# Kernel tuning notes

Hardware: AMD Instinct MI355X
Metric: run time of the kernel (lower is better)

The kernel has to match this reference:

```python
import math
import jax, jax.numpy as jnp
import numpy as np

B, N, D, NH, DFF, DRAW, TMAX = 4, 1024, 512, 8, 2048, 32, 2
DK = D // NH
LN_EPS = 1e-5


def bayes_linear(x, w_mu, w_rho, b_mu, b_rho):
    # closed-form mean/variance of a variational linear layer
    w_sig = jax.nn.softplus(w_rho)
    b_sig = jax.nn.softplus(b_rho)
    mean = x @ w_mu.T + b_mu
    var = (x * x) @ (w_sig * w_sig).T + b_sig * b_sig
    return mean, var


def layer_norm(x, g, b):
    mu = jnp.mean(x, axis=-1, keepdims=True)
    v = jnp.var(x, axis=-1, keepdims=True)
    return (x - mu) / jnp.sqrt(v + LN_EPS) * g + b


def gelu_deriv(x):
    phi = 0.5 * (1.0 + jax.lax.erf(x / math.sqrt(2.0)))
    pdf = jnp.exp(-0.5 * x * x) / math.sqrt(2.0 * math.pi)
    return phi + x * pdf


def attention(x, x_raw, w_mu, w_rho, b_mu, b_rho, log_sigma_f, log_length):
    Bb, Nn, Dd = x.shape
    qm, _ = bayes_linear(x, w_mu[0], w_rho[0], b_mu[0], b_rho[0])
    km, _ = bayes_linear(x, w_mu[1], w_rho[1], b_mu[1], b_rho[1])
    vm, vv = bayes_linear(x, w_mu[2], w_rho[2], b_mu[2], b_rho[2])

    def heads(t):
        return t.reshape(Bb, Nn, NH, DK).transpose(0, 2, 1, 3)  # [B,H,N,dk]

    Q, K, V, Vv = heads(qm), heads(km), heads(vm), heads(vv)
    scores = jnp.einsum('bhnd,bhmd->bhnm', Q, K) / math.sqrt(DK)
    # RBF kernel on raw inputs, per head; dist2 via |x|^2+|x'|^2-2xx' (no [B,N,N,d] diff tensor)
    sq = jnp.sum(x_raw * x_raw, axis=-1)
    dist2 = jnp.maximum(sq[:, :, None] + sq[:, None, :] - 2.0 * jnp.einsum('bnd,bmd->bnm', x_raw, x_raw), 0.0)
    sigma_f2 = jnp.exp(2.0 * log_sigma_f)
    length2 = jnp.exp(2.0 * log_length)
    rbf = sigma_f2[None, :, None, None] * jnp.exp(-dist2[:, None, :, :] / (2.0 * length2[None, :, None, None]))
    attn = jax.nn.softmax(scores + rbf, axis=-1)
    ctx = jnp.einsum('bhnm,bhmd->bhnd', attn, V).transpose(0, 2, 1, 3).reshape(Bb, Nn, Dd)
    vta = jnp.einsum('bhnm,bhmd->bhnd', attn * attn, Vv).transpose(0, 2, 1, 3).reshape(Bb, Nn, Dd)
    om, ovp = bayes_linear(ctx, w_mu[3], w_rho[3], b_mu[3], b_rho[3])
    return om, ovp + vta


def ffn(x, w1_mu, w1_rho, b1_mu, b1_rho, w2_mu, w2_rho, b2_mu, b2_rho):
    hm, hv = bayes_linear(x, w1_mu, w1_rho, b1_mu, b1_rho)
    am = jax.nn.gelu(hm, approximate=False)
    av = gelu_deriv(hm) ** 2 * hv
    om, ovd = bayes_linear(am, w2_mu, w2_rho, b2_mu, b2_rho)
    w2_sig = jax.nn.softplus(w2_rho)
    vc = av @ (w2_mu * w2_mu + w2_sig * w2_sig).T
    return om, ovd + vc


def cascade(H, H_var, tau_k, x_raw, attn_w_mu, attn_w_rho, attn_b_mu, attn_b_rho,
            w1_mu, w1_rho, b1_mu, b1_rho, w2_mu, w2_rho, b2_mu, b2_rho,
            ln1_g, ln1_b, ln2_g, ln2_b, log_sigma_f, log_length, log_gammas):
    g = jax.nn.softplus(log_gammas)
    g1, g2, g3, g4 = g[0], g[1], g[2], g[3]
    alpha = g1 / (g1 + g2)  # E[alpha] (inference path)
    beta = g3 / (g3 + g4)
    Va = g1 * g2 / ((g1 + g2) ** 2 * (g1 + g2 + 1.0))
    Vb = g3 * g4 / ((g3 + g4) ** 2 * (g3 + g4 + 1.0))
    done = jnp.asarray(False)
    for _ in range(TMAX):
        n1 = layer_norm(H, ln1_g, ln1_b)
        am, avar = attention(n1, x_raw, attn_w_mu, attn_w_rho, attn_b_mu, attn_b_rho, log_sigma_f, log_length)
        Hb = H + am
        n2 = layer_norm(Hb, ln2_g, ln2_b)
        fm, fvar = ffn(n2, w1_mu, w1_rho, b1_mu, b1_rho, w2_mu, w2_rho, b2_mu, b2_rho)
        F_out = Hb + fm
        F_var = avar + fvar
        Hn = alpha * H + beta * F_out
        Hvn = (alpha ** 2) * H_var + (beta ** 2) * F_var + Va * H * H + Vb * F_out * F_out + Va * H_var + Vb * F_var
        H = jnp.where(done, H, Hn)
        H_var = jnp.where(done, H_var, Hvn)
        done = done | (jnp.mean(H_var) <= tau_k)  # early-exit freeze
    return H, H_var


def setup_inputs() -> dict:
    key = jax.random.key(0)
    ks = jax.random.split(key, 8)
    inp = {
        'H': jax.random.normal(ks[0], (B, N, D), jnp.float32),
        'H_var': jax.random.uniform(ks[1], (B, N, D), jnp.float32) * 0.1,
        'x_raw': jax.random.normal(ks[2], (B, N, DRAW), jnp.float32) * 0.15,
        'tau_k': jnp.zeros((), jnp.float32),
        'attn_w_mu': jax.random.normal(ks[3], (4, D, D), jnp.float32) / math.sqrt(D),
        'attn_w_rho': jnp.full((4, D, D), -3.0, jnp.float32),
        'attn_b_mu': jnp.zeros((4, D), jnp.float32),
        'attn_b_rho': jnp.full((4, D), -3.0, jnp.float32),
        'w1_mu': jax.random.normal(ks[4], (DFF, D), jnp.float32) / math.sqrt(D),
        'w1_rho': jnp.full((DFF, D), -3.0, jnp.float32),
        'b1_mu': jnp.zeros((DFF,), jnp.float32),
        'b1_rho': jnp.full((DFF,), -3.0, jnp.float32),
        'w2_mu': jax.random.normal(ks[5], (D, DFF), jnp.float32) / math.sqrt(DFF),
        'w2_rho': jnp.full((D, DFF), -3.0, jnp.float32),
        'b2_mu': jnp.zeros((D,), jnp.float32),
        'b2_rho': jnp.full((D,), -3.0, jnp.float32),
        'ln1_g': jnp.ones((D,), jnp.float32),
        'ln1_b': jnp.zeros((D,), jnp.float32),
        'ln2_g': jnp.ones((D,), jnp.float32),
        'ln2_b': jnp.zeros((D,), jnp.float32),
        'log_sigma_f': jnp.zeros((NH,), jnp.float32),
        'log_length': jnp.zeros((NH,), jnp.float32),
        'log_gammas': jnp.ones((4,), jnp.float32),
    }
    return inp


def reference(H, H_var, x_raw, tau_k, attn_w_mu, attn_w_rho, attn_b_mu, attn_b_rho,
              w1_mu, w1_rho, b1_mu, b1_rho, w2_mu, w2_rho, b2_mu, b2_rho,
              ln1_g, ln1_b, ln2_g, ln2_b, log_sigma_f, log_length, log_gammas):
    return cascade(H, H_var, tau_k, x_raw, attn_w_mu, attn_w_rho, attn_b_mu, attn_b_rho,
                   w1_mu, w1_rho, b1_mu, b1_rho, w2_mu, w2_rho, b2_mu, b2_rho,
                   ln1_g, ln1_b, ln2_g, ln2_b, log_sigma_f, log_length, log_gammas)
```

## Files before the change

### kernel.cpp

```cpp
#include <hip/hip_runtime.h>
#include <math.h>


#define Bx   4
#define Nx   1024
#define Dx   512
#define NHx  8
#define DFFx 2048

static constexpr size_t BN  = (size_t)Bx * Nx;
static constexpr size_t BND = BN * Dx;
static constexpr size_t BNF = BN * DFFx;
static constexpr int    DD  = Dx * Dx;
static constexpr int    DF  = DFFx * Dx;

typedef __attribute__((ext_vector_type(8))) short bf16x8;
typedef __attribute__((ext_vector_type(4))) float f32x4;

__device__ __forceinline__ float sp_(float x) {
  return x > 20.f ? x : log1pf(expf(x));
}
__device__ __forceinline__ unsigned short f2b(float f) {
  unsigned u = __float_as_uint(f);
  unsigned r = (u + 0x7fffu + ((u >> 16) & 1u)) >> 16;
  return (unsigned short)r;
}
__device__ __forceinline__ float b2f(unsigned short v) {
  return __uint_as_float((unsigned)v << 16);
}
__device__ __forceinline__ void gld16(const void* g, void* l) {
  __builtin_amdgcn_global_load_lds(
      (const __attribute__((address_space(1))) unsigned int*)g,
      (__attribute__((address_space(3))) unsigned int*)l, 16, 0, 0);
}

__global__ __launch_bounds__(256) void cvt_weights(
    const float* __restrict__ aw_mu, const float* __restrict__ aw_rho,
    const float* __restrict__ w1_mu, const float* __restrict__ w1_rho,
    const float* __restrict__ w2_mu, const float* __restrict__ w2_rho,
    unsigned short* __restrict__ aw_bf,
    unsigned short* __restrict__ wvvar_bf,
    unsigned short* __restrict__ wovar_bf,
    unsigned short* __restrict__ w1_bf, unsigned short* __restrict__ w1var_bf,
    unsigned short* __restrict__ w2_bf, unsigned short* __restrict__ w2var_bf,
    unsigned short* __restrict__ w2comb_bf)
{
  int i = blockIdx.x * 256 + threadIdx.x;
  if (i < 4 * DD) {
    aw_bf[i] = f2b(aw_mu[i]);
  } else if (i < 6 * DD) {
    int j = i - 4 * DD;
    if (j < DD) { float s = sp_(aw_rho[2 * DD + j]); wvvar_bf[j] = f2b(s * s); }
    else { int k = j - DD; float s = sp_(aw_rho[3 * DD + k]); wovar_bf[k] = f2b(s * s); }
  } else if (i < 6 * DD + DF) {
    int j = i - 6 * DD;
    w1_bf[j] = f2b(w1_mu[j]);
  } else if (i < 6 * DD + 2 * DF) {
    int j = i - 6 * DD - DF;
    float s = sp_(w1_rho[j]); w1var_bf[j] = f2b(s * s);
  } else if (i < 6 * DD + 3 * DF) {
    int j = i - 6 * DD - 2 * DF;
    float m = w2_mu[j];
    float s = sp_(w2_rho[j]); float v = s * s;
    w2_bf[j] = f2b(m);
    w2var_bf[j] = f2b(v);
    w2comb_bf[j] = f2b(m * m + v);
  }
}

__global__ __launch_bounds__(256) void prep_small(
    const float* __restrict__ attn_b_rho, const float* __restrict__ b1_rho,
    const float* __restrict__ b2_rho, const float* __restrict__ xraw,
    float* __restrict__ bv2, float* __restrict__ bo2,
    float* __restrict__ b1v, float* __restrict__ b2v,
    float* __restrict__ sqb)
{
  int i = blockIdx.x * 256 + threadIdx.x;
  if (i < 512) {
    float s = sp_(attn_b_rho[1024 + i]); bv2[i] = s * s;
  } else if (i < 1024) {
    int k = i - 512;
    float s = sp_(attn_b_rho[1536 + k]); bo2[k] = s * s;
  } else if (i < 3072) {
    int k = i - 1024;
    float s = sp_(b1_rho[k]); b1v[k] = s * s;
  } else if (i < 3584) {
    int k = i - 3072;
    float s = sp_(b2_rho[k]); b2v[k] = s * s;
  } else if (i < 3584 + (int)BN) {
    int row = i - 3584;
    const float* x = xraw + (size_t)row * 32;
    float acc = 0.f;
    #pragma unroll
    for (int t = 0; t < 32; t++) acc += x[t] * x[t];
    sqb[row] = acc;
  }
}

__global__ __launch_bounds__(256) void gram_rbf(
    const float* __restrict__ xraw, const float* __restrict__ sqb,
    const float* __restrict__ lsf, const float* __restrict__ lll,
    unsigned short* __restrict__ rbf)
{
  const int nt = blockIdx.x, mt = blockIdx.y, b = blockIdx.z;
  __shared__ float xn[64][36];
  __shared__ float xm[64][36];
  __shared__ float sn[64], sm[64];
  const int tid = threadIdx.x;
  for (int q = tid; q < 512; q += 256) {
    int rr = q >> 3, cc = (q & 7) << 2;
    *(float4*)&xn[rr][cc] =
        *(const float4*)(xraw + ((size_t)b * Nx + nt * 64 + rr) * 32 + cc);
    *(float4*)&xm[rr][cc] =
        *(const float4*)(xraw + ((size_t)b * Nx + mt * 64 + rr) * 32 + cc);
  }
  if (tid < 64) {
    sn[tid] = sqb[(size_t)b * Nx + nt * 64 + tid];
    sm[tid] = sqb[(size_t)b * Nx + mt * 64 + tid];
  }
  __syncthreads();
  const int r = tid >> 2, j = tid & 3;
  float dd[16];
  #pragma unroll
  for (int i = 0; i < 16; i++) {
    int mm = j * 16 + i;
    float g = 0.f;
    #pragma unroll
    for (int t = 0; t < 32; t++) g += xn[r][t] * xm[mm][t];
    dd[i] = fmaxf(sn[r] + sm[mm] - 2.f * g, 0.f);
  }
  const int n = nt * 64 + r;
  #pragma unroll
  for (int h = 0; h < NHx; h++) {
    float sf2 = expf(2.f * lsf[h]);
    float i2l = 0.5f * expf(-2.f * lll[h]);
    unsigned short tmp[16];
    #pragma unroll
    for (int i = 0; i < 16; i++) tmp[i] = f2b(sf2 * expf(-dd[i] * i2l));
    unsigned short* dst =
        rbf + ((size_t)(h * Bx + b) * Nx + n) * Nx + mt * 64 + j * 16;
    *(uint4*)dst = *(const uint4*)&tmp[0];
    *(uint4*)(dst + 8) = *(const uint4*)&tmp[8];
  }
}

__global__ __launch_bounds__(256) void layernorm_bf(
    const float* __restrict__ X, const float* __restrict__ g,
    const float* __restrict__ bta,
    unsigned short* __restrict__ Y, unsigned short* __restrict__ Ysq)
{
  const int row = blockIdx.x;
  const float* x = X + (size_t)row * Dx;
  const int tid = threadIdx.x;
  float v0 = x[tid], v1 = x[tid + 256];
  float s = v0 + v1;
  float ss = v0 * v0 + v1 * v1;
  #pragma unroll
  for (int o = 32; o > 0; o >>= 1) {
    s += __shfl_down(s, o);
    ss += __shfl_down(ss, o);
  }
  __shared__ float ps[4], pss[4];
  const int w = tid >> 6;
  if ((tid & 63) == 0) { ps[w] = s; pss[w] = ss; }
  __syncthreads();
  float S = ps[0] + ps[1] + ps[2] + ps[3];
  float SS = pss[0] + pss[1] + pss[2] + pss[3];
  float mean = S * (1.f / 512.f);
  float var = fmaxf(SS * (1.f / 512.f) - mean * mean, 0.f);
  float inv = rsqrtf(var + 1e-5f);
  float y0 = (v0 - mean) * inv * g[tid] + bta[tid];
  float y1 = (v1 - mean) * inv * g[tid + 256] + bta[tid + 256];
  Y[(size_t)row * Dx + tid] = f2b(y0);
  Y[(size_t)row * Dx + tid + 256] = f2b(y1);
  Ysq[(size_t)row * Dx + tid] = f2b(y0 * y0);
  Ysq[(size_t)row * Dx + tid + 256] = f2b(y1 * y1);
}

struct GD {
  const unsigned short* A;
  const unsigned short* W;
  const float* bias;
  const float* add_in;
  void* C;
  int N;
  int trans;
};

template <bool HALFM, bool OUTBF>
__global__ __launch_bounds__(256) void gemm_mf(
    GD d0, GD d1, GD d2, int M, int K, int ldc)
{
  const GD d = (blockIdx.z == 0) ? d0 : ((blockIdx.z == 1) ? d1 : d2);
  const int n0 = blockIdx.x * 128;
  if (n0 >= d.N) return;
  constexpr int BM = HALFM ? 64 : 128;
  const int m0 = blockIdx.y * BM;

  __shared__ short As0[BM * 32];
  __shared__ short As1[BM * 32];
  __shared__ short Ws0[128 * 32];
  __shared__ short Ws1[128 * 32];

  const int tid = threadIdx.x;
  const int lane = tid & 63;
  const int wv = tid >> 6;
  const int wr = wv >> 1, wc = wv & 1;
  const int fr = lane & 15;
  const int fk = (lane >> 4) * 8;

  const int rowA = m0 + (tid >> 2);
  const int rowW = n0 + (tid >> 2);
  const int colc = (tid & 3) * 8;
  const unsigned short* gA0 = d.A + (size_t)rowA * K + colc;
  const unsigned short* gA1 = gA0 + (size_t)64 * K;
  const unsigned short* gW0 = d.W + (size_t)rowW * K + colc;
  const unsigned short* gW1 = gW0 + (size_t)64 * K;
  short* lA00 = &As0[tid * 8];
  short* lA01 = &As1[tid * 8];
  short* lA10 = &As0[(tid + 256) * 8];
  short* lA11 = &As1[(tid + 256) * 8];
  short* lW00 = &Ws0[tid * 8];
  short* lW01 = &Ws1[tid * 8];
  short* lW10 = &Ws0[(tid + 256) * 8];
  short* lW11 = &Ws1[(tid + 256) * 8];

  constexpr int MI = BM / 32;
  f32x4 acc[MI][4] = {};

  for (int k0 = 0; k0 < K; k0 += 64) {
    gld16(gA0 + k0, lA00);
    gld16(gA0 + k0 + 32, lA01);
    if (!HALFM) {
      gld16(gA1 + k0, lA10);
      gld16(gA1 + k0 + 32, lA11);
    }
    gld16(gW0 + k0, lW00);
    gld16(gW0 + k0 + 32, lW01);
    gld16(gW1 + k0, lW10);
    gld16(gW1 + k0 + 32, lW11);
    __syncthreads();

    {
      bf16x8 af[MI], bfr[4];
      #pragma unroll
      for (int mi = 0; mi < MI; mi++)
        af[mi] = *(const bf16x8*)&As0[(wr * (BM / 2) + mi * 16 + fr) * 32 + fk];
      #pragma unroll
      for (int ni = 0; ni < 4; ni++)
        bfr[ni] = *(const bf16x8*)&Ws0[(wc * 64 + ni * 16 + fr) * 32 + fk];
      #pragma unroll
      for (int mi = 0; mi < MI; mi++)
        #pragma unroll
        for (int ni = 0; ni < 4; ni++)
          acc[mi][ni] = __builtin_amdgcn_mfma_f32_16x16x32_bf16(
              af[mi], bfr[ni], acc[mi][ni], 0, 0, 0);
    }
    {
      bf16x8 af[MI], bfr[4];
      #pragma unroll
      for (int mi = 0; mi < MI; mi++)
        af[mi] = *(const bf16x8*)&As1[(wr * (BM / 2) + mi * 16 + fr) * 32 + fk];
      #pragma unroll
      for (int ni = 0; ni < 4; ni++)
        bfr[ni] = *(const bf16x8*)&Ws1[(wc * 64 + ni * 16 + fr) * 32 + fk];
      #pragma unroll
      for (int mi = 0; mi < MI; mi++)
        #pragma unroll
        for (int ni = 0; ni < 4; ni++)
          acc[mi][ni] = __builtin_amdgcn_mfma_f32_16x16x32_bf16(
              af[mi], bfr[ni], acc[mi][ni], 0, 0, 0);
    }
    __syncthreads();
  }

  const int quad = lane >> 4;
  #pragma unroll
  for (int mi = 0; mi < MI; mi++) {
    #pragma unroll
    for (int ni = 0; ni < 4; ni++) {
      int col = n0 + wc * 64 + ni * 16 + fr;
      if (col >= d.N) continue;
      float bv = d.bias ? d.bias[col] : 0.f;
      int rowb = m0 + wr * (BM / 2) + mi * 16 + quad * 4;
      if (d.trans) {
        ushort4 o;
        o.x = f2b(acc[mi][ni][0] + bv);
        o.y = f2b(acc[mi][ni][1] + bv);
        o.z = f2b(acc[mi][ni][2] + bv);
        o.w = f2b(acc[mi][ni][3] + bv);
        *(ushort4*)&((unsigned short*)d.C)[(size_t)col * M + rowb] = o;
      } else {
        #pragma unroll
        for (int r = 0; r < 4; r++) {
          float v = acc[mi][ni][r] + bv;
          if (d.add_in) v += d.add_in[(size_t)(rowb + r) * ldc + col];
          if (OUTBF)
            ((unsigned short*)d.C)[(size_t)(rowb + r) * ldc + col] = f2b(v);
          else
            ((float*)d.C)[(size_t)(rowb + r) * ldc + col] = v;
        }
      }
    }
  }
}

__global__ __launch_bounds__(256) void flash_mfma(
    const unsigned short* __restrict__ QK,
    const unsigned short* __restrict__ VT,
    const unsigned short* __restrict__ rbf,
    unsigned short* __restrict__ ctx_bf, unsigned short* __restrict__ ctxsq_bf,
    float* __restrict__ vta)
{
  const int qt = blockIdx.x, h = blockIdx.y, b = blockIdx.z;
  const int q0 = qt * 64;
  const int tid = threadIdx.x;
  const int w = tid >> 6;
  const int lane = tid & 63;
  const int fr = lane & 15;
  const int quad = lane >> 4;

  __shared__ unsigned short Kt[64 * 72];
  __shared__ unsigned short VtT[64 * 72];
  __shared__ unsigned short VvT[64 * 72];
  __shared__ unsigned short Pt[64 * 72];
  __shared__ unsigned short P2t[64 * 72];
  __shared__ float lred[4][16];

  bf16x8 qa0, qa1;
  {
    const unsigned short* qp =
        QK + ((size_t)(b * Nx + q0 + w * 16 + fr)) * 1024 + h * 64 + quad * 8;
    qa0 = *(const bf16x8*)qp;
    qa1 = *(const bf16x8*)(qp + 32);
  }

  float lsum[4] = {0.f, 0.f, 0.f, 0.f};
  f32x4 accO[4] = {};
  f32x4 accW[4] = {};

  const unsigned short* kg = QK + ((size_t)b * Nx) * 1024 + 512 + h * 64;
  const unsigned short* vg = VT + (size_t)(h * 64) * BN + b * Nx;
  const unsigned short* ug = VT + (size_t)(512 + h * 64) * BN + b * Nx;
  const unsigned short* rb =
      rbf + ((size_t)(h * Bx + b) * Nx + q0 + w * 16 + quad * 4) * Nx;

  const int a0 = tid >> 3;
  const int c8 = (tid & 7) * 8;

  uint4 pk0, pk1, pv0, pv1, pu0, pu1;
  pk0 = *(const uint4*)(kg + (size_t)a0 * 1024 + c8);
  pk1 = *(const uint4*)(kg + (size_t)(a0 + 32) * 1024 + c8);
  pv0 = *(const uint4*)(vg + (size_t)a0 * BN + c8);
  pv1 = *(const uint4*)(vg + (size_t)(a0 + 32) * BN + c8);
  pu0 = *(const uint4*)(ug + (size_t)a0 * BN + c8);
  pu1 = *(const uint4*)(ug + (size_t)(a0 + 32) * BN + c8);

  for (int mt = 0; mt < 16; mt++) {
    __syncthreads();
    *(uint4*)&Kt[a0 * 72 + c8] = pk0;
    *(uint4*)&Kt[(a0 + 32) * 72 + c8] = pk1;
    *(uint4*)&VtT[a0 * 72 + c8] = pv0;
    *(uint4*)&VtT[(a0 + 32) * 72 + c8] = pv1;
    *(uint4*)&VvT[a0 * 72 + c8] = pu0;
    *(uint4*)&VvT[(a0 + 32) * 72 + c8] = pu1;
    __syncthreads();

    if (mt + 1 < 16) {
      const int n1 = (mt + 1) * 64;
      pk0 = *(const uint4*)(kg + (size_t)(n1 + a0) * 1024 + c8);
      pk1 = *(const uint4*)(kg + (size_t)(n1 + a0 + 32) * 1024 + c8);
      pv0 = *(const uint4*)(vg + (size_t)a0 * BN + n1 + c8);
      pv1 = *(const uint4*)(vg + (size_t)(a0 + 32) * BN + n1 + c8);
      pu0 = *(const uint4*)(ug + (size_t)a0 * BN + n1 + c8);
      pu1 = *(const uint4*)(ug + (size_t)(a0 + 32) * BN + n1 + c8);
    }

    f32x4 accS[4] = {};
    #pragma unroll
    for (int ni = 0; ni < 4; ni++) {
      bf16x8 b0 = *(const bf16x8*)&Kt[(ni * 16 + fr) * 72 + quad * 8];
      bf16x8 b1 = *(const bf16x8*)&Kt[(ni * 16 + fr) * 72 + 32 + quad * 8];
      accS[ni] = __builtin_amdgcn_mfma_f32_16x16x32_bf16(qa0, b0, accS[ni], 0, 0, 0);
      accS[ni] = __builtin_amdgcn_mfma_f32_16x16x32_bf16(qa1, b1, accS[ni], 0, 0, 0);
    }

    const int m0 = mt * 64;
    #pragma unroll
    for (int reg = 0; reg < 4; reg++) {
      const unsigned short* rr = rb + (size_t)reg * Nx + m0;
      int rowb = (w * 16 + quad * 4 + reg) * 72;
      #pragma unroll
      for (int ni = 0; ni < 4; ni++) {
        float pv = expf(accS[ni][reg] * 0.125f + b2f(rr[ni * 16 + fr]));
        lsum[reg] += pv;
        Pt[rowb + ni * 16 + fr] = f2b(pv);
        P2t[rowb + ni * 16 + fr] = f2b(pv * pv);
      }
    }
    __syncthreads();

    #pragma unroll
    for (int ks = 0; ks < 2; ks++) {
      bf16x8 pa  = *(const bf16x8*)&Pt[(w * 16 + fr) * 72 + ks * 32 + quad * 8];
      bf16x8 p2a = *(const bf16x8*)&P2t[(w * 16 + fr) * 72 + ks * 32 + quad * 8];
      #pragma unroll
      for (int ni = 0; ni < 4; ni++) {
        bf16x8 vb = *(const bf16x8*)&VtT[(ni * 16 + fr) * 72 + ks * 32 + quad * 8];
        bf16x8 ub = *(const bf16x8*)&VvT[(ni * 16 + fr) * 72 + ks * 32 + quad * 8];
        accO[ni] = __builtin_amdgcn_mfma_f32_16x16x32_bf16(vb, pa, accO[ni], 0, 0, 0);
        accW[ni] = __builtin_amdgcn_mfma_f32_16x16x32_bf16(ub, p2a, accW[ni], 0, 0, 0);
      }
    }
  }

  #pragma unroll
  for (int reg = 0; reg < 4; reg++) {
    float t = lsum[reg];
    t += __shfl_xor(t, 1);
    t += __shfl_xor(t, 2);
    t += __shfl_xor(t, 4);
    t += __shfl_xor(t, 8);
    lsum[reg] = t;
  }
  if (fr == 0) {
    #pragma unroll
    for (int reg = 0; reg < 4; reg++) lred[w][quad * 4 + reg] = lsum[reg];
  }
  __syncthreads();
  float invl = 1.f / lred[w][fr];
  float invl2 = invl * invl;

  size_t row = (size_t)b * Nx + q0 + w * 16 + fr;
  #pragma unroll
  for (int ni = 0; ni < 4; ni++) {
    int dkb = h * 64 + ni * 16 + quad * 4;
    ushort4 oc, oc2;
    float4 ov;
    float c0 = accO[ni][0] * invl, c1 = accO[ni][1] * invl;
    float c2 = accO[ni][2] * invl, c3 = accO[ni][3] * invl;
    oc.x = f2b(c0); oc.y = f2b(c1); oc.z = f2b(c2); oc.w = f2b(c3);
    oc2.x = f2b(c0 * c0); oc2.y = f2b(c1 * c1);
    oc2.z = f2b(c2 * c2); oc2.w = f2b(c3 * c3);
    ov.x = accW[ni][0] * invl2; ov.y = accW[ni][1] * invl2;
    ov.z = accW[ni][2] * invl2; ov.w = accW[ni][3] * invl2;
    *(ushort4*)&ctx_bf[row * Dx + dkb] = oc;
    *(ushort4*)&ctxsq_bf[row * Dx + dkb] = oc2;
    *(float4*)&vta[row * Dx + dkb] = ov;
  }
}

__global__ __launch_bounds__(256) void gelu_triple(
    unsigned short* __restrict__ hm, unsigned short* __restrict__ hv,
    unsigned short* __restrict__ am2)
{
  size_t i8 = ((size_t)blockIdx.x * 256 + threadIdx.x) * 8;
  uint4 hm8 = *(const uint4*)&hm[i8];
  uint4 hv8 = *(const uint4*)&hv[i8];
  const unsigned short* ms = (const unsigned short*)&hm8;
  const unsigned short* vs = (const unsigned short*)&hv8;
  unsigned short oa[8], ob[8], oc[8];
  #pragma unroll
  for (int j = 0; j < 8; j++) {
    float x = b2f(ms[j]);
    float phi = 0.5f * (1.f + erff(x * 0.70710678118654752f));
    float pdf = expf(-0.5f * x * x) * 0.39894228040143268f;
    float am = x * phi;
    float gd = phi + x * pdf;
    oa[j] = f2b(am);
    ob[j] = f2b(am * am);
    oc[j] = f2b(gd * gd * b2f(vs[j]));
  }
  *(uint4*)&hm[i8] = *(const uint4*)&oa[0];
  *(uint4*)&am2[i8] = *(const uint4*)&ob[0];
  *(uint4*)&hv[i8] = *(const uint4*)&oc[0];
}

__global__ __launch_bounds__(256) void combine_k(
    const float* __restrict__ Hin, const float* __restrict__ Hvin,
    float* __restrict__ Hout, float* __restrict__ Hvout,
    const float* __restrict__ F, const float* __restrict__ avar,
    const float* __restrict__ ovd, const float* __restrict__ vc,
    const float* __restrict__ lg)
{
  size_t i = ((size_t)blockIdx.x * 256 + threadIdx.x) * 4;
  float g1 = sp_(lg[0]), g2 = sp_(lg[1]), g3 = sp_(lg[2]), g4 = sp_(lg[3]);
  float s12 = g1 + g2, s34 = g3 + g4;
  float alpha = g1 / s12, beta = g3 / s34;
  float Va = g1 * g2 / (s12 * s12 * (s12 + 1.f));
  float Vb = g3 * g4 / (s34 * s34 * (s34 + 1.f));
  float4 h4 = *(const float4*)&Hin[i];
  float4 hv4 = *(const float4*)&Hvin[i];
  float4 F4 = *(const float4*)&F[i];
  float4 a4 = *(const float4*)&avar[i];
  float4 o4 = *(const float4*)&ovd[i];
  float4 c4 = *(const float4*)&vc[i];
  float* hp = (float*)&h4; float* vp = (float*)&hv4;
  const float* Fp = (const float*)&F4; const float* ap = (const float*)&a4;
  const float* op = (const float*)&o4; const float* cp = (const float*)&c4;
  float4 ho, vo;
  float* hop = (float*)&ho; float* vop = (float*)&vo;
  #pragma unroll
  for (int j = 0; j < 4; j++) {
    float h = hp[j], hv = vp[j];
    float Fm = Fp[j];
    float Fv = ap[j] + op[j] + cp[j];
    hop[j] = alpha * h + beta * Fm;
    vop[j] = alpha * alpha * hv + beta * beta * Fv + Va * h * h + Vb * Fm * Fm +
             Va * hv + Vb * Fv;
  }
  *(float4*)&Hout[i] = ho;
  *(float4*)&Hvout[i] = vo;
}

extern "C" void kernel_launch(void* const* d_in, const int* in_sizes, int n_in,
                              void* d_out, int out_size, void* d_ws, size_t ws_size,
                              hipStream_t stream)
{
  const float* H_in   = (const float*)d_in[0];
  const float* Hv_in  = (const float*)d_in[1];
  const float* x_raw  = (const float*)d_in[2];
  const float* aw_mu  = (const float*)d_in[4];
  const float* aw_rho = (const float*)d_in[5];
  const float* ab_mu  = (const float*)d_in[6];
  const float* ab_rho = (const float*)d_in[7];
  const float* w1_mu  = (const float*)d_in[8];
  const float* w1_rho = (const float*)d_in[9];
  const float* b1_mu  = (const float*)d_in[10];
  const float* b1_rho = (const float*)d_in[11];
  const float* w2_mu  = (const float*)d_in[12];
  const float* w2_rho = (const float*)d_in[13];
  const float* b2_mu  = (const float*)d_in[14];
  const float* b2_rho = (const float*)d_in[15];
  const float* ln1_g  = (const float*)d_in[16];
  const float* ln1_b  = (const float*)d_in[17];
  const float* ln2_g  = (const float*)d_in[18];
  const float* ln2_b  = (const float*)d_in[19];
  const float* lsf    = (const float*)d_in[20];
  const float* lll    = (const float*)d_in[21];
  const float* lgam   = (const float*)d_in[22];

  float* Hout = (float*)d_out;
  float* Hvar = (float*)d_out + BND;

  float* ws = (float*)d_ws;
  size_t off = 0;
  auto allocf = [&](size_t n) {
    float* p = ws + off; off += (n + 7) & ~(size_t)7; return p;
  };
  auto allocus = [&](size_t n) {
    return (unsigned short*)allocf((n + 1) / 2);
  };
  unsigned short* rbf = allocus((size_t)NHx * Bx * Nx * Nx);
  float* vta = allocf(BND);
  float* Hb  = allocf(BND);
  float* ovd = allocf(BND);
  float* vc  = allocf(BND);
  unsigned short* QKb = allocus(BN * 1024);
  unsigned short* VTb = allocus((size_t)1024 * BN);
  unsigned short* lnA = allocus(BND);
  unsigned short* lnB = allocus(BND);
  unsigned short* hm_bf  = allocus(BNF);
  unsigned short* hv_bf  = allocus(BNF);
  unsigned short* am2_bf = allocus(BNF);
  unsigned short* aw_bf     = allocus(4 * DD);
  unsigned short* wvvar_bf  = allocus(DD);
  unsigned short* wovar_bf  = allocus(DD);
  unsigned short* w1_bf     = allocus(DF);
  unsigned short* w1var_bf  = allocus(DF);
  unsigned short* w2_bf     = allocus(DF);
  unsigned short* w2var_bf  = allocus(DF);
  unsigned short* w2comb_bf = allocus(DF);
  float* bv2 = allocf(512);
  float* bo2 = allocf(512);
  float* b1v = allocf(2048);
  float* b2v = allocf(512);
  float* sqb = allocf(BN);
  (void)ws_size; (void)in_sizes; (void)n_in; (void)out_size;

  cvt_weights<<<(6 * DD + 3 * DF + 255) / 256, 256, 0, stream>>>(
      aw_mu, aw_rho, w1_mu, w1_rho, w2_mu, w2_rho,
      aw_bf, wvvar_bf, wovar_bf, w1_bf, w1var_bf, w2_bf, w2var_bf, w2comb_bf);
  prep_small<<<(3584 + (int)BN + 255) / 256, 256, 0, stream>>>(
      ab_rho, b1_rho, b2_rho, x_raw, bv2, bo2, b1v, b2v, sqb);
  gram_rbf<<<dim3(16, 16, Bx), 256, 0, stream>>>(x_raw, sqb, lsf, lll, rbf);

  const int M = (int)BN;
  GD dz = {nullptr, nullptr, nullptr, nullptr, nullptr, 0, 0};

  const float* Hsrc  = H_in;
  const float* Hvsrc = Hv_in;

  for (int t = 0; t < 2; t++) {
    layernorm_bf<<<(int)BN, 256, 0, stream>>>(Hsrc, ln1_g, ln1_b, lnA, lnB);
    {
      GD dqk = {lnA, aw_bf, ab_mu, nullptr, (void*)QKb, 1024, 0};
      GD dv  = {lnA, aw_bf + 2 * (size_t)DD, ab_mu + 1024, nullptr,
                (void*)VTb, 512, 1};
      GD dvv = {lnB, wvvar_bf, bv2, nullptr,
                (void*)(VTb + (size_t)512 * BN), 512, 1};
      gemm_mf<false, true><<<dim3(8, 32, 3), 256, 0, stream>>>(
          dqk, dv, dvv, M, 512, 1024);
    }
    flash_mfma<<<dim3(Nx / 64, NHx, Bx), 256, 0, stream>>>(
        QKb, VTb, rbf, lnA, lnB, vta);
    {
      GD d_om = {lnA, aw_bf + 3 * (size_t)DD, ab_mu + 1536, Hsrc, (void*)Hb,
                 512, 0};
      GD d_ov = {lnB, wovar_bf, bo2, vta, (void*)vta, 512, 0};
      gemm_mf<true, false><<<dim3(4, 64, 2), 256, 0, stream>>>(
          d_om, d_ov, dz, M, 512, 512);
    }

    layernorm_bf<<<(int)BN, 256, 0, stream>>>(Hb, ln2_g, ln2_b, lnA, lnB);
    {
      GD d_hm = {lnA, w1_bf, b1_mu, nullptr, (void*)hm_bf, 2048, 0};
      GD d_hv = {lnB, w1var_bf, b1v, nullptr, (void*)hv_bf, 2048, 0};
      gemm_mf<false, true><<<dim3(16, 32, 2), 256, 0, stream>>>(
          d_hm, d_hv, dz, M, 512, 2048);
    }
    gelu_triple<<<(int)(BNF / (256 * 8)), 256, 0, stream>>>(hm_bf, hv_bf, am2_bf);
    {
      GD d_fm  = {hm_bf, w2_bf, b2_mu, Hb, (void*)Hb, 512, 0};
      GD d_ovd = {am2_bf, w2var_bf, b2v, nullptr, (void*)ovd, 512, 0};
      GD d_vc  = {hv_bf, w2comb_bf, nullptr, nullptr, (void*)vc, 512, 0};
      gemm_mf<true, false><<<dim3(4, 64, 3), 256, 0, stream>>>(
          d_fm, d_ovd, d_vc, M, 2048, 512);
    }
    combine_k<<<(int)(BND / (256 * 4)), 256, 0, stream>>>(
        Hsrc, Hvsrc, Hout, Hvar, Hb, vta, ovd, vc, lgam);

    Hsrc = Hout;
    Hvsrc = Hvar;
  }
}
```

Baseline: 613.7 us.

## Register-prefetch GEMM tiles, square P in registers, merge prep kernels and residual adds

The GEMM main loop now prefetches the next K tile from global memory into registers while the current tile is used for MFMA, instead of issuing direct global-to-LDS loads followed by a barrier. The attention kernel drops the separate P² shared buffer and squares the P fragments in registers after loading them. The two prep kernels are merged into one launch, and the vta term is folded into the FFN variance GEMM epilogue, so combine_k reads one fewer buffer. These changes target load latency, LDS traffic, launch overhead and memory reads, at the cost of more registers per thread and a different rounding path for P².

```diff
diff --git a/kernel.cpp b/kernel.cpp
--- a/kernel.cpp
+++ b/kernel.cpp
@@ -28,22 +28,31 @@
 __device__ __forceinline__ float b2f(unsigned short v) {
   return __uint_as_float((unsigned)v << 16);
 }
-__device__ __forceinline__ void gld16(const void* g, void* l) {
-  __builtin_amdgcn_global_load_lds(
-      (const __attribute__((address_space(1))) unsigned int*)g,
-      (__attribute__((address_space(3))) unsigned int*)l, 16, 0, 0);
+__device__ __forceinline__ bf16x8 sq8(bf16x8 a) {
+  bf16x8 r;
+  #pragma unroll
+  for (int j = 0; j < 8; j++) {
+    float f = b2f((unsigned short)a[j]);
+    r[j] = (short)f2b(f * f);
+  }
+  return r;
 }
 
 __global__ __launch_bounds__(256) void cvt_weights(
     const float* __restrict__ aw_mu, const float* __restrict__ aw_rho,
     const float* __restrict__ w1_mu, const float* __restrict__ w1_rho,
     const float* __restrict__ w2_mu, const float* __restrict__ w2_rho,
+    const float* __restrict__ attn_b_rho, const float* __restrict__ b1_rho,
+    const float* __restrict__ b2_rho, const float* __restrict__ xraw,
     unsigned short* __restrict__ aw_bf,
     unsigned short* __restrict__ wvvar_bf,
     unsigned short* __restrict__ wovar_bf,
     unsigned short* __restrict__ w1_bf, unsigned short* __restrict__ w1var_bf,
     unsigned short* __restrict__ w2_bf, unsigned short* __restrict__ w2var_bf,
-    unsigned short* __restrict__ w2comb_bf)
+    unsigned short* __restrict__ w2comb_bf,
+    float* __restrict__ bv2, float* __restrict__ bo2,
+    float* __restrict__ b1v, float* __restrict__ b2v,
+    float* __restrict__ sqb)
 {
   int i = blockIdx.x * 256 + threadIdx.x;
   if (i < 4 * DD) {
@@ -65,35 +74,27 @@
     w2_bf[j] = f2b(m);
     w2var_bf[j] = f2b(v);
     w2comb_bf[j] = f2b(m * m + v);
-  }
-}
-
-__global__ __launch_bounds__(256) void prep_small(
-    const float* __restrict__ attn_b_rho, const float* __restrict__ b1_rho,
-    const float* __restrict__ b2_rho, const float* __restrict__ xraw,
-    float* __restrict__ bv2, float* __restrict__ bo2,
-    float* __restrict__ b1v, float* __restrict__ b2v,
-    float* __restrict__ sqb)
-{
-  int i = blockIdx.x * 256 + threadIdx.x;
-  if (i < 512) {
-    float s = sp_(attn_b_rho[1024 + i]); bv2[i] = s * s;
-  } else if (i < 1024) {
-    int k = i - 512;
-    float s = sp_(attn_b_rho[1536 + k]); bo2[k] = s * s;
-  } else if (i < 3072) {
-    int k = i - 1024;
-    float s = sp_(b1_rho[k]); b1v[k] = s * s;
-  } else if (i < 3584) {
-    int k = i - 3072;
-    float s = sp_(b2_rho[k]); b2v[k] = s * s;
-  } else if (i < 3584 + (int)BN) {
-    int row = i - 3584;
-    const float* x = xraw + (size_t)row * 32;
-    float acc = 0.f;
-    #pragma unroll
-    for (int t = 0; t < 32; t++) acc += x[t] * x[t];
-    sqb[row] = acc;
+  } else {
+    int j = i - (6 * DD + 3 * DF);
+    if (j < 512) {
+      float s = sp_(attn_b_rho[1024 + j]); bv2[j] = s * s;
+    } else if (j < 1024) {
+      int k = j - 512;
+      float s = sp_(attn_b_rho[1536 + k]); bo2[k] = s * s;
+    } else if (j < 3072) {
+      int k = j - 1024;
+      float s = sp_(b1_rho[k]); b1v[k] = s * s;
+    } else if (j < 3584) {
+      int k = j - 3072;
+      float s = sp_(b2_rho[k]); b2v[k] = s * s;
+    } else if (j < 3584 + (int)BN) {
+      int row = j - 3584;
+      const float* x = xraw + (size_t)row * 32;
+      float acc = 0.f;
+      #pragma unroll
+      for (int t = 0; t < 32; t++) acc += x[t] * x[t];
+      sqb[row] = acc;
+    }
   }
 }
 
@@ -228,18 +229,47 @@
   constexpr int MI = BM / 32;
   f32x4 acc[MI][4] = {};
 
+  uint4 ra0, ra1, ra2, ra3, rw0, rw1, rw2, rw3;
+  {
+    ra0 = *(const uint4*)(gA0);
+    ra1 = *(const uint4*)(gA0 + 32);
+    if (!HALFM) {
+      ra2 = *(const uint4*)(gA1);
+      ra3 = *(const uint4*)(gA1 + 32);
+    }
+    rw0 = *(const uint4*)(gW0);
+    rw1 = *(const uint4*)(gW0 + 32);
+    rw2 = *(const uint4*)(gW1);
+    rw3 = *(const uint4*)(gW1 + 32);
+  }
+
   for (int k0 = 0; k0 < K; k0 += 64) {
-    gld16(gA0 + k0, lA00);
-    gld16(gA0 + k0 + 32, lA01);
+    __syncthreads();
+    *(uint4*)lA00 = ra0;
+    *(uint4*)lA01 = ra1;
     if (!HALFM) {
-      gld16(gA1 + k0, lA10);
-      gld16(gA1 + k0 + 32, lA11);
-    }
-    gld16(gW0 + k0, lW00);
-    gld16(gW0 + k0 + 32, lW01);
-    gld16(gW1 + k0, lW10);
-    gld16(gW1 + k0 + 32, lW11);
+      *(uint4*)lA10 = ra2;
+      *(uint4*)lA11 = ra3;
+    }
+    *(uint4*)lW00 = rw0;
+    *(uint4*)lW01 = rw1;
+    *(uint4*)lW10 = rw2;
+    *(uint4*)lW11 = rw3;
     __syncthreads();
+
+    if (k0 + 64 < K) {
+      int kn = k0 + 64;
+      ra0 = *(const uint4*)(gA0 + kn);
+      ra1 = *(const uint4*)(gA0 + kn + 32);
+      if (!HALFM) {
+        ra2 = *(const uint4*)(gA1 + kn);
+        ra3 = *(const uint4*)(gA1 + kn + 32);
+      }
+      rw0 = *(const uint4*)(gW0 + kn);
+      rw1 = *(const uint4*)(gW0 + kn + 32);
+      rw2 = *(const uint4*)(gW1 + kn);
+      rw3 = *(const uint4*)(gW1 + kn + 32);
+    }
 
     {
       bf16x8 af[MI], bfr[4];
@@ -271,7 +301,6 @@
           acc[mi][ni] = __builtin_amdgcn_mfma_f32_16x16x32_bf16(
               af[mi], bfr[ni], acc[mi][ni], 0, 0, 0);
     }
-    __syncthreads();
   }
 
   const int quad = lane >> 4;
@@ -324,7 +353,6 @@
   __shared__ unsigned short VtT[64 * 72];
   __shared__ unsigned short VvT[64 * 72];
   __shared__ unsigned short Pt[64 * 72];
-  __shared__ unsigned short P2t[64 * 72];
   __shared__ float lred[4][16];
 
   bf16x8 qa0, qa1;
@@ -395,7 +423,6 @@
         float pv = expf(accS[ni][reg] * 0.125f + b2f(rr[ni * 16 + fr]));
         lsum[reg] += pv;
         Pt[rowb + ni * 16 + fr] = f2b(pv);
-        P2t[rowb + ni * 16 + fr] = f2b(pv * pv);
       }
     }
     __syncthreads();
@@ -403,7 +430,7 @@
     #pragma unroll
     for (int ks = 0; ks < 2; ks++) {
       bf16x8 pa  = *(const bf16x8*)&Pt[(w * 16 + fr) * 72 + ks * 32 + quad * 8];
-      bf16x8 p2a = *(const bf16x8*)&P2t[(w * 16 + fr) * 72 + ks * 32 + quad * 8];
+      bf16x8 p2a = sq8(pa);
       #pragma unroll
       for (int ni = 0; ni < 4; ni++) {
         bf16x8 vb = *(const bf16x8*)&VtT[(ni * 16 + fr) * 72 + ks * 32 + quad * 8];
@@ -479,9 +506,8 @@
 __global__ __launch_bounds__(256) void combine_k(
     const float* __restrict__ Hin, const float* __restrict__ Hvin,
     float* __restrict__ Hout, float* __restrict__ Hvout,
-    const float* __restrict__ F, const float* __restrict__ avar,
-    const float* __restrict__ ovd, const float* __restrict__ vc,
-    const float* __restrict__ lg)
+    const float* __restrict__ F, const float* __restrict__ fva,
+    const float* __restrict__ vc, const float* __restrict__ lg)
 {
   size_t i = ((size_t)blockIdx.x * 256 + threadIdx.x) * 4;
   float g1 = sp_(lg[0]), g2 = sp_(lg[1]), g3 = sp_(lg[2]), g4 = sp_(lg[3]);
@@ -492,19 +518,18 @@
   float4 h4 = *(const float4*)&Hin[i];
   float4 hv4 = *(const float4*)&Hvin[i];
   float4 F4 = *(const float4*)&F[i];
-  float4 a4 = *(const float4*)&avar[i];
-  float4 o4 = *(const float4*)&ovd[i];
+  float4 a4 = *(const float4*)&fva[i];
   float4 c4 = *(const float4*)&vc[i];
   float* hp = (float*)&h4; float* vp = (float*)&hv4;
   const float* Fp = (const float*)&F4; const float* ap = (const float*)&a4;
-  const float* op = (const float*)&o4; const float* cp = (const float*)&c4;
+  const float* cp = (const float*)&c4;
   float4 ho, vo;
   float* hop = (float*)&ho; float* vop = (float*)&vo;
   #pragma unroll
   for (int j = 0; j < 4; j++) {
     float h = hp[j], hv = vp[j];
     float Fm = Fp[j];
-    float Fv = ap[j] + op[j] + cp[j];
+    float Fv = ap[j] + cp[j];
     hop[j] = alpha * h + beta * Fm;
     vop[j] = alpha * alpha * hv + beta * beta * Fv + Va * h * h + Vb * Fm * Fm +
              Va * hv + Vb * Fv;
@@ -554,7 +579,7 @@
   unsigned short* rbf = allocus((size_t)NHx * Bx * Nx * Nx);
   float* vta = allocf(BND);
   float* Hb  = allocf(BND);
-  float* ovd = allocf(BND);
+  float* fva = allocf(BND);
   float* vc  = allocf(BND);
   unsigned short* QKb = allocus(BN * 1024);
   unsigned short* VTb = allocus((size_t)1024 * BN);
@@ -578,11 +603,14 @@
   float* sqb = allocf(BN);
   (void)ws_size; (void)in_sizes; (void)n_in; (void)out_size;
 
-  cvt_weights<<<(6 * DD + 3 * DF + 255) / 256, 256, 0, stream>>>(
-      aw_mu, aw_rho, w1_mu, w1_rho, w2_mu, w2_rho,
-      aw_bf, wvvar_bf, wovar_bf, w1_bf, w1var_bf, w2_bf, w2var_bf, w2comb_bf);
-  prep_small<<<(3584 + (int)BN + 255) / 256, 256, 0, stream>>>(
-      ab_rho, b1_rho, b2_rho, x_raw, bv2, bo2, b1v, b2v, sqb);
+  {
+    int tot = 6 * DD + 3 * DF + 3584 + (int)BN;
+    cvt_weights<<<(tot + 255) / 256, 256, 0, stream>>>(
+        aw_mu, aw_rho, w1_mu, w1_rho, w2_mu, w2_rho,
+        ab_rho, b1_rho, b2_rho, x_raw,
+        aw_bf, wvvar_bf, wovar_bf, w1_bf, w1var_bf, w2_bf, w2var_bf,
+        w2comb_bf, bv2, bo2, b1v, b2v, sqb);
+  }
   gram_rbf<<<dim3(16, 16, Bx), 256, 0, stream>>>(x_raw, sqb, lsf, lll, rbf);
 
   const int M = (int)BN;
@@ -622,13 +650,13 @@
     gelu_triple<<<(int)(BNF / (256 * 8)), 256, 0, stream>>>(hm_bf, hv_bf, am2_bf);
     {
       GD d_fm  = {hm_bf, w2_bf, b2_mu, Hb, (void*)Hb, 512, 0};
-      GD d_ovd = {am2_bf, w2var_bf, b2v, nullptr, (void*)ovd, 512, 0};
+      GD d_ovd = {am2_bf, w2var_bf, b2v, vta, (void*)fva, 512, 0};
       GD d_vc  = {hv_bf, w2comb_bf, nullptr, nullptr, (void*)vc, 512, 0};
       gemm_mf<true, false><<<dim3(4, 64, 3), 256, 0, stream>>>(
           d_fm, d_ovd, d_vc, M, 2048, 512);
     }
     combine_k<<<(int)(BND / (256 * 4)), 256, 0, stream>>>(
-        Hsrc, Hvsrc, Hout, Hvar, Hb, vta, ovd, vc, lgam);
+        Hsrc, Hvsrc, Hout, Hvar, Hb, fva, vc, lgam);
 
     Hsrc = Hout;
     Hvsrc = Hvar;
```

Result: slower. 653.0 us (+6.4%).
